# Optimization experiments

Measured on AMD Instinct MI355X. Metric: run time of the kernel, lower is better.

## Reference

```python
import jax, jax.numpy as jnp
import numpy as np

B, LAT, HID = 256, 20, 128
G, BIN = 25000, 25       # original_dim, bin_size
C = 7                    # max_cp + 1 copy-number states
GB = G // BIN            # rho head output dim


def setup_inputs() -> dict:
    key = jax.random.key(0)
    ks = jax.random.split(key, 16)
    s = 0.01  # TruncatedNormal(stddev=0.01) init
    return {
        "z": jax.random.normal(ks[0], (B, LAT), jnp.float32),
        "w0": jax.random.normal(ks[1], (LAT, HID), jnp.float32) * s,
        "b0": jnp.zeros((HID,), jnp.float32),
        "g0": jnp.ones((HID,), jnp.float32),
        "be0": jnp.zeros((HID,), jnp.float32),
        "m0": jax.random.normal(ks[2], (HID,), jnp.float32) * 0.1,
        "v0": jax.random.uniform(ks[3], (HID,), jnp.float32, 0.5, 1.5),
        "w1": jax.random.normal(ks[4], (HID, HID), jnp.float32) * s,
        "b1": jnp.zeros((HID,), jnp.float32),
        "g1": jnp.ones((HID,), jnp.float32),
        "be1": jnp.zeros((HID,), jnp.float32),
        "m1": jax.random.normal(ks[5], (HID,), jnp.float32) * 0.1,
        "v1": jax.random.uniform(ks[6], (HID,), jnp.float32, 0.5, 1.5),
        "wr": jax.random.normal(ks[7], (HID, G), jnp.float32) * s,
        "br": jnp.zeros((G,), jnp.float32),
        "wd": jax.random.normal(ks[8], (HID, G), jnp.float32) * s,
        "bd": jnp.zeros((G,), jnp.float32),
        "wrho": jax.random.normal(ks[9], (C, HID, GB), jnp.float32) * s,
        "brho": jnp.zeros((C, GB), jnp.float32),
        "ws": jax.random.normal(ks[10], (G,), jnp.float32) * 0.05,
        "bs": jax.random.normal(ks[11], (G,), jnp.float32) * 0.05,
    }


def reference(z, w0, b0, g0, be0, m0, v0, w1, b1, g1, be1, m1, v1,
              wr, br, wd, bd, wrho, brho, ws, bs):
    BN_EPS = 1e-3
    EPS = 1e-20
    TEMP = 0.1

    def bn(x, gamma, beta, mean, var):
        # inference-mode BatchNormalization(momentum=0.01, epsilon=0.001)
        return (x - mean) * jax.lax.rsqrt(var + BN_EPS) * gamma + beta

    # FullyConnLayer x2: Dense -> BN -> ReLU
    x = jax.nn.relu(bn(z @ w0 + b0, g0, be0, m0, v0))
    x = jax.nn.relu(bn(x @ w1 + b1, g1, be1, m1, v1))

    theta = jnp.exp(x @ wr + br)        # [B, G]
    pi_drop = x @ wd + bd               # [B, G]

    # max_cp+1 rho Dense heads fused into a single batched GEMM -> [C, B, GB]
    rho = jnp.einsum('bh,cho->cbo', x, wrho) + brho[:, None, :]
    rho = jax.nn.softmax(rho, axis=0)   # softmax over copy-number states

    # GumbelSoftmaxSampling: stack(axis=1) -> [B, C, GB]
    rho_b = jnp.transpose(rho, (1, 0, 2))
    gene_rho = jnp.repeat(rho_b, BIN, axis=-1)        # [B, C, G]
    pi = jnp.transpose(gene_rho, (0, 2, 1))           # [B, G, C]

    u = jax.random.uniform(jax.random.key(42), pi.shape, jnp.float32)
    gnoise = -jnp.log(-jnp.log(u + EPS) + EPS)
    y = jax.nn.softmax((jnp.log(pi + EPS) + gnoise) / TEMP, axis=-1)
    y_hard = (y == jnp.max(y, axis=-1, keepdims=True)).astype(jnp.float32)
    y = jax.lax.stop_gradient(y_hard - y) + y         # straight-through

    # multiply by copy-number index matrix and reduce -> expected/sampled copy
    cvals = jnp.arange(C, dtype=jnp.float32)
    sample = jnp.sum(y * cvals, axis=-1)              # [B, G]

    # ScaleLayer: sigmoid(x * w + b)
    mu = jax.nn.sigmoid(sample * ws + bs)             # [B, G]
    return (mu, theta, pi_drop, sample, pi)
```

## Files before the change

### kernel.cpp

```cpp
#include <hip/hip_runtime.h>

#define B 256
#define LAT 20
#define HID 128
#define G 25000
#define GB 1000
#define NC 7

typedef __attribute__((ext_vector_type(8))) short short8;
typedef __attribute__((ext_vector_type(4))) float f32x4;

__device__ __forceinline__ unsigned short f2bf(float f) {
  unsigned int u = __float_as_uint(f);
  u += 0x7fffu + ((u >> 16) & 1u);
  return (unsigned short)(u >> 16);
}

__device__ __forceinline__ unsigned int threefry_xor(unsigned int idx) {
  unsigned int x0 = 0u;
  unsigned int x1 = idx + 42u;
#define TF_R(r) { x0 += x1; x1 = (x1 << r) | (x1 >> (32 - r)); x1 ^= x0; }
  TF_R(13) TF_R(15) TF_R(26) TF_R(6)
  x0 += 42u;          x1 += 0x1BD11BF1u;
  TF_R(17) TF_R(29) TF_R(16) TF_R(24)
  x0 += 0x1BD11BF0u;  x1 += 2u;
  TF_R(13) TF_R(15) TF_R(26) TF_R(6)
   x1 += 45u;
  TF_R(17) TF_R(29) TF_R(16) TF_R(24)
  x0 += 42u;          x1 += 0x1BD11BF4u;
  TF_R(13) TF_R(15) TF_R(26) TF_R(6)
  x0 += 0x1BD11BF0u;  x1 += 5u;
#undef TF_R
  return x0 ^ x1;
}

__global__ void k_mlp(const float* __restrict__ z,  const float* __restrict__ w0,
                      const float* __restrict__ b0, const float* __restrict__ g0,
                      const float* __restrict__ be0, const float* __restrict__ m0,
                      const float* __restrict__ v0,
                      const float* __restrict__ w1, const float* __restrict__ b1,
                      const float* __restrict__ g1, const float* __restrict__ be1,
                      const float* __restrict__ m1, const float* __restrict__ v1,
                      double* __restrict__ x64, unsigned short* __restrict__ x_bf) {
  __shared__ double xs[HID];
  const int b = blockIdx.x, h = threadIdx.x;
  double acc = (double)b0[h];
  for (int k = 0; k < LAT; ++k)
    acc += (double)z[b * LAT + k] * (double)w0[k * HID + h];
  double y = (acc - (double)m0[h]) * (1.0 / sqrt((double)v0[h] + 1e-3)) * (double)g0[h]
             + (double)be0[h];
  y = y > 0.0 ? y : 0.0;
  xs[h] = y;
  __syncthreads();
  double a1 = (double)b1[h];
  for (int k = 0; k < HID; ++k)
    a1 += xs[k] * (double)w1[k * HID + h];
  double y1 = (a1 - (double)m1[h]) * (1.0 / sqrt((double)v1[h] + 1e-3)) * (double)g1[h]
              + (double)be1[h];
  y1 = y1 > 0.0 ? y1 : 0.0;
  x64[h * B + b] = y1;
  x_bf[b * HID + h] = f2bf((float)y1);
}

__global__ void k_trans(const float* __restrict__ wr, const float* __restrict__ wd,
                        unsigned short* __restrict__ wrT, unsigned short* __restrict__ wdT) {
  __shared__ float t[64][65];
  const float* src = blockIdx.z ? wd : wr;
  unsigned short* dst = blockIdx.z ? wdT : wrT;
  const int g0 = blockIdx.x * 64, h0 = blockIdx.y * 64;
#pragma unroll
  for (int i = 0; i < 16; ++i) {
    int f = i * 256 + threadIdx.x;
    int hl = f >> 6, gl = f & 63;
    int g = g0 + gl;
    t[hl][gl] = (g < G) ? src[(h0 + hl) * G + g] : 0.f;
  }
  __syncthreads();
#pragma unroll
  for (int i = 0; i < 16; ++i) {
    int f = i * 256 + threadIdx.x;
    int gl = f >> 6, hl = f & 63;
    int g = g0 + gl;
    if (g < G) dst[(size_t)g * HID + h0 + hl] = f2bf(t[hl][gl]);
  }
}

__global__ void k_rho(const double* __restrict__ x64, const float* __restrict__ wrho,
                      const float* __restrict__ brho,
                      float* __restrict__ pi32, float* __restrict__ lp32,
                      double* __restrict__ lp64) {
  __shared__ float wl[NC * HID * 16];
  const int o0 = blockIdx.x * 16, bB = blockIdx.y * 64;
  for (int i = threadIdx.x; i < NC * HID * 16; i += 256) {
    int ol = i & 15, hh = (i >> 4) & 127, c = i >> 11;
    int o = o0 + ol;
    wl[i] = (o < GB) ? wrho[(c * HID + hh) * GB + o] : 0.f;
  }
  __syncthreads();
  const int lane = threadIdx.x & 63, w = threadIdx.x >> 6;
  const int b = bB + lane;
  double acc[4][NC];
#pragma unroll
  for (int p = 0; p < 4; ++p) {
    int o = o0 + w + 4 * p; int oc = o < GB ? o : GB - 1;
#pragma unroll
    for (int c = 0; c < NC; ++c) acc[p][c] = (double)brho[c * GB + oc];
  }
  for (int h = 0; h < HID; ++h) {
    double xv = x64[h * B + b];
#pragma unroll
    for (int p = 0; p < 4; ++p) {
#pragma unroll
      for (int c = 0; c < NC; ++c)
        acc[p][c] += xv * (double)wl[(c * HID + h) * 16 + (w + 4 * p)];
    }
  }
#pragma unroll
  for (int p = 0; p < 4; ++p) {
    int o = o0 + w + 4 * p;
    if (o >= GB) continue;
    double m = acc[p][0];
#pragma unroll
    for (int c = 1; c < NC; ++c) m = fmax(m, acc[p][c]);
    double e[NC], s = 0.0;
#pragma unroll
    for (int c = 0; c < NC; ++c) { e[c] = exp(acc[p][c] - m); s += e[c]; }
    size_t base = ((size_t)o * B + b) * 8;
#pragma unroll
    for (int c = 0; c < NC; ++c) {
      double pi = e[c] / s;
      double lp = log(pi + 1e-20);
      pi32[base + c] = (float)pi;
      lp32[base + c] = (float)lp;
      lp64[base + c] = lp;
    }
  }
}

__global__ __launch_bounds__(256) void k_main(
    const unsigned short* __restrict__ x_bf,
    const unsigned short* __restrict__ wrT, const unsigned short* __restrict__ wdT,
    const float* __restrict__ br, const float* __restrict__ bd,
    const float* __restrict__ wsc, const float* __restrict__ bsc,
    const float* __restrict__ pi32, const float* __restrict__ lp32,
    const double* __restrict__ lp64, float* __restrict__ out) {
  const int tid = threadIdx.x;
  const int wv = tid >> 6, lane = tid & 63;
  const int n = lane & 15, quad = lane >> 4;
  const int gt = wv & 1, btbase = (wv >> 1) * 8;
  const int g = blockIdx.x * 32 + gt * 16 + n;
  const bool gvalid = g < G;
  const int gcl = gvalid ? g : G - 1;
  const float brv = br[gcl], bdv = bd[gcl], wsv = wsc[gcl], bsv = bsc[gcl];
  const int o = gcl / 25;
  const float* lpb = lp32 + ((size_t)o * B) * 8;
  const float* pib = pi32 + ((size_t)o * B) * 8;
  const double* lqb = lp64 + ((size_t)o * B) * 8;

  short8 fr[4], fd[4];
  {
    const short8* p1 = (const short8*)(wrT + (size_t)gcl * HID + quad * 8);
    const short8* p2 = (const short8*)(wdT + (size_t)gcl * HID + quad * 8);
#pragma unroll
    for (int ks = 0; ks < 4; ++ks) { fr[ks] = p1[ks * 4]; fd[ks] = p2[ks * 4]; }
  }

  for (int bti = 0; bti < 8; ++bti) {
    const int bt = btbase + bti;
    const short8* xp = (const short8*)(x_bf + (size_t)(bt * 16 + n) * HID + quad * 8);
    f32x4 accr = {0.f, 0.f, 0.f, 0.f}, accd = {0.f, 0.f, 0.f, 0.f};
#pragma unroll
    for (int ks = 0; ks < 4; ++ks) {
      short8 fa = xp[ks * 4];
      accr = __builtin_amdgcn_mfma_f32_16x16x32_bf16(fa, fr[ks], accr, 0, 0, 0);
      accd = __builtin_amdgcn_mfma_f32_16x16x32_bf16(fa, fd[ks], accd, 0, 0, 0);
    }
#pragma unroll
    for (int i = 0; i < 4; ++i) {
      const int b = bt * 16 + quad * 4 + i;
      const float th = expf(accr[i] + brv);
      const float pd = accd[i] + bdv;
      const float* lpp = lpb + (size_t)b * 8;
      f32x4 l0 = *(const f32x4*)lpp;
      f32x4 l1 = *(const f32x4*)(lpp + 4);
      float lpv[8];
      lpv[0] = l0[0]; lpv[1] = l0[1]; lpv[2] = l0[2]; lpv[3] = l0[3];
      lpv[4] = l1[0]; lpv[5] = l1[1]; lpv[6] = l1[2]; lpv[7] = l1[3];
      unsigned int bits[NC];
      const unsigned int idx0 = (unsigned int)b * 175000u + (unsigned int)g * 7u;
      float best = -3.4e38f, sec = -3.4e38f; int arg = 0;
#pragma unroll
      for (int c = 0; c < NC; ++c) {
        unsigned int bb = threefry_xor(idx0 + (unsigned int)c);
        bits[c] = bb;
        float uf = __uint_as_float((bb >> 9) | 0x3f800000u) - 1.0f;
        float gn = -logf(-logf(uf + 1e-20f) + 1e-20f);
        float mv = lpv[c] + gn;
        if (mv > best) { sec = best; best = mv; arg = c; }
        else if (mv > sec) sec = mv;
      }
      int s = arg;
      if (best - sec < 2e-3f) {
        const double* lq = lqb + (size_t)b * 8;
        double lv[NC], bestd = -1e300;
#pragma unroll
        for (int c = 0; c < NC; ++c) {
          float uf = __uint_as_float((bits[c] >> 9) | 0x3f800000u) - 1.0f;
          double gn = -log(-log((double)uf + 1e-20) + 1e-20);
          lv[c] = lq[c] + gn;
          bestd = fmax(bestd, lv[c]);
        }
        s = 0;
#pragma unroll
        for (int c = 0; c < NC; ++c) if (lv[c] == bestd) s += c;
      }
      if (gvalid) {
        const float smp = (float)s;
        const float mu = 1.f / (1.f + expf(-(smp * wsv + bsv)));
        const size_t og = (size_t)b * G + g;
        out[og] = mu;
        out[6400000 + og] = th;
        out[12800000 + og] = pd;
        out[19200000 + og] = smp;
        const float* pip = pib + (size_t)b * 8;
        f32x4 p0 = *(const f32x4*)pip;
        f32x4 p1v = *(const f32x4*)(pip + 4);
        const size_t pbo = 25600000 + og * 7;
        out[pbo + 0] = p0[0]; out[pbo + 1] = p0[1]; out[pbo + 2] = p0[2]; out[pbo + 3] = p0[3];
        out[pbo + 4] = p1v[0]; out[pbo + 5] = p1v[1]; out[pbo + 6] = p1v[2];
      }
    }
  }
}

extern "C" void kernel_launch(void* const* d_in, const int* in_sizes, int n_in,
                              void* d_out, int out_size, void* d_ws, size_t ws_size,
                              hipStream_t stream) {
  const float* z   = (const float*)d_in[0];
  const float* w0  = (const float*)d_in[1];
  const float* b0  = (const float*)d_in[2];
  const float* g0  = (const float*)d_in[3];
  const float* be0 = (const float*)d_in[4];
  const float* m0  = (const float*)d_in[5];
  const float* v0  = (const float*)d_in[6];
  const float* w1  = (const float*)d_in[7];
  const float* b1  = (const float*)d_in[8];
  const float* g1  = (const float*)d_in[9];
  const float* be1 = (const float*)d_in[10];
  const float* m1  = (const float*)d_in[11];
  const float* v1  = (const float*)d_in[12];
  const float* wr  = (const float*)d_in[13];
  const float* br  = (const float*)d_in[14];
  const float* wd  = (const float*)d_in[15];
  const float* bd  = (const float*)d_in[16];
  const float* wrho= (const float*)d_in[17];
  const float* brho= (const float*)d_in[18];
  const float* wsc = (const float*)d_in[19];
  const float* bsc = (const float*)d_in[20];

  char* ws = (char*)d_ws;
  unsigned short* x_bf = (unsigned short*)(ws);
  double* x64          = (double*)(ws + 65536);
  unsigned short* wrT  = (unsigned short*)(ws + 327680);
  unsigned short* wdT  = (unsigned short*)(ws + 6727680);
  float* pi32          = (float*)(ws + 13127680);
  float* lp32          = (float*)(ws + 21319680);
  double* lp64         = (double*)(ws + 29511680);
  float* out = (float*)d_out;

  k_mlp<<<dim3(256), dim3(128), 0, stream>>>(z, w0, b0, g0, be0, m0, v0,
                                             w1, b1, g1, be1, m1, v1, x64, x_bf);
  k_trans<<<dim3(391, 2, 2), dim3(256), 0, stream>>>(wr, wd, wrT, wdT);
  k_rho<<<dim3(63, 4), dim3(256), 0, stream>>>(x64, wrho, brho, pi32, lp32, lp64);
  k_main<<<dim3(782), dim3(256), 0, stream>>>(x_bf, wrT, wdT, br, bd, wsc, bsc,
                                              pi32, lp32, lp64, out);
}
```

Measured before the change: 634.3 us.

## Retile rho and main kernels, switch rho buffers to channel-major layout

k_rho now gives each block 4 output bins instead of 16, so the grid grows from 252 to 1000 blocks and each thread keeps 7 rather than 28 double accumulators. The rho intermediates move from a padded [o][b][8] layout to a channel-major [o][c][b] layout, making the per-channel stores and loads contiguous across batch lanes. k_main adds a second grid dimension that splits the batch tiles, doubling block count and halving the loop per wave. The outer log in the Gumbel noise becomes the fast __logf intrinsic, which may shift near-tie argmax decisions, though a double-precision fallback still handles near ties.

Result: faster. 550.7 us (-13.2%).

```diff
diff --git a/kernel.cpp b/kernel.cpp
--- a/kernel.cpp
+++ b/kernel.cpp
@@ -85,55 +85,43 @@
   }
 }
 
-__global__ void k_rho(const double* __restrict__ x64, const float* __restrict__ wrho,
-                      const float* __restrict__ brho,
+__global__ __launch_bounds__(256) void k_rho(const double* __restrict__ x64,
+                      const float* __restrict__ wrho, const float* __restrict__ brho,
                       float* __restrict__ pi32, float* __restrict__ lp32,
                       double* __restrict__ lp64) {
-  __shared__ float wl[NC * HID * 16];
-  const int o0 = blockIdx.x * 16, bB = blockIdx.y * 64;
-  for (int i = threadIdx.x; i < NC * HID * 16; i += 256) {
-    int ol = i & 15, hh = (i >> 4) & 127, c = i >> 11;
-    int o = o0 + ol;
-    wl[i] = (o < GB) ? wrho[(c * HID + hh) * GB + o] : 0.f;
+  __shared__ float wl[NC * HID * 4];
+  const int o0 = blockIdx.x * 4, bB = blockIdx.y * 64;
+  for (int i = threadIdx.x; i < NC * HID * 4; i += 256) {
+    int ol = i & 3, rest = i >> 2;
+    int c = rest >> 7, h = rest & 127;
+    wl[i] = wrho[(c * HID + h) * GB + o0 + ol];
   }
   __syncthreads();
-  const int lane = threadIdx.x & 63, w = threadIdx.x >> 6;
-  const int b = bB + lane;
-  double acc[4][NC];
-#pragma unroll
-  for (int p = 0; p < 4; ++p) {
-    int o = o0 + w + 4 * p; int oc = o < GB ? o : GB - 1;
-#pragma unroll
-    for (int c = 0; c < NC; ++c) acc[p][c] = (double)brho[c * GB + oc];
-  }
+  const int lane = threadIdx.x & 63, ol = threadIdx.x >> 6;
+  const int b = bB + lane, o = o0 + ol;
+  double acc[NC];
+#pragma unroll
+  for (int c = 0; c < NC; ++c) acc[c] = (double)brho[c * GB + o];
   for (int h = 0; h < HID; ++h) {
     double xv = x64[h * B + b];
 #pragma unroll
-    for (int p = 0; p < 4; ++p) {
-#pragma unroll
-      for (int c = 0; c < NC; ++c)
-        acc[p][c] += xv * (double)wl[(c * HID + h) * 16 + (w + 4 * p)];
-    }
-  }
-#pragma unroll
-  for (int p = 0; p < 4; ++p) {
-    int o = o0 + w + 4 * p;
-    if (o >= GB) continue;
-    double m = acc[p][0];
-#pragma unroll
-    for (int c = 1; c < NC; ++c) m = fmax(m, acc[p][c]);
-    double e[NC], s = 0.0;
-#pragma unroll
-    for (int c = 0; c < NC; ++c) { e[c] = exp(acc[p][c] - m); s += e[c]; }
-    size_t base = ((size_t)o * B + b) * 8;
-#pragma unroll
-    for (int c = 0; c < NC; ++c) {
-      double pi = e[c] / s;
-      double lp = log(pi + 1e-20);
-      pi32[base + c] = (float)pi;
-      lp32[base + c] = (float)lp;
-      lp64[base + c] = lp;
-    }
+    for (int c = 0; c < NC; ++c)
+      acc[c] += xv * (double)wl[(c * HID + h) * 4 + ol];
+  }
+  double m = acc[0];
+#pragma unroll
+  for (int c = 1; c < NC; ++c) m = fmax(m, acc[c]);
+  double e[NC], s = 0.0;
+#pragma unroll
+  for (int c = 0; c < NC; ++c) { e[c] = exp(acc[c] - m); s += e[c]; }
+  const size_t base = (size_t)o * (NC * B) + b;
+#pragma unroll
+  for (int c = 0; c < NC; ++c) {
+    double pi = e[c] / s;
+    double lp = log(pi + 1e-20);
+    pi32[base + c * B] = (float)pi;
+    lp32[base + c * B] = (float)lp;
+    lp64[base + c * B] = lp;
   }
 }
 
@@ -147,15 +135,16 @@
   const int tid = threadIdx.x;
   const int wv = tid >> 6, lane = tid & 63;
   const int n = lane & 15, quad = lane >> 4;
-  const int gt = wv & 1, btbase = (wv >> 1) * 8;
+  const int gt = wv & 1;
+  const int btbase = blockIdx.y * 8 + (wv >> 1) * 4;
   const int g = blockIdx.x * 32 + gt * 16 + n;
   const bool gvalid = g < G;
   const int gcl = gvalid ? g : G - 1;
   const float brv = br[gcl], bdv = bd[gcl], wsv = wsc[gcl], bsv = bsc[gcl];
   const int o = gcl / 25;
-  const float* lpb = lp32 + ((size_t)o * B) * 8;
-  const float* pib = pi32 + ((size_t)o * B) * 8;
-  const double* lqb = lp64 + ((size_t)o * B) * 8;
+  const float*  lpb = lp32 + (size_t)o * (NC * B);
+  const float*  pib = pi32 + (size_t)o * (NC * B);
+  const double* lqb = lp64 + (size_t)o * (NC * B);
 
   short8 fr[4], fd[4];
   {
@@ -165,7 +154,7 @@
     for (int ks = 0; ks < 4; ++ks) { fr[ks] = p1[ks * 4]; fd[ks] = p2[ks * 4]; }
   }
 
-  for (int bti = 0; bti < 8; ++bti) {
+  for (int bti = 0; bti < 4; ++bti) {
     const int bt = btbase + bti;
     const short8* xp = (const short8*)(x_bf + (size_t)(bt * 16 + n) * HID + quad * 8);
     f32x4 accr = {0.f, 0.f, 0.f, 0.f}, accd = {0.f, 0.f, 0.f, 0.f};
@@ -180,12 +169,9 @@
       const int b = bt * 16 + quad * 4 + i;
       const float th = expf(accr[i] + brv);
       const float pd = accd[i] + bdv;
-      const float* lpp = lpb + (size_t)b * 8;
-      f32x4 l0 = *(const f32x4*)lpp;
-      f32x4 l1 = *(const f32x4*)(lpp + 4);
-      float lpv[8];
-      lpv[0] = l0[0]; lpv[1] = l0[1]; lpv[2] = l0[2]; lpv[3] = l0[3];
-      lpv[4] = l1[0]; lpv[5] = l1[1]; lpv[6] = l1[2]; lpv[7] = l1[3];
+      float lpv[NC];
+#pragma unroll
+      for (int c = 0; c < NC; ++c) lpv[c] = lpb[c * B + b];
       unsigned int bits[NC];
       const unsigned int idx0 = (unsigned int)b * 175000u + (unsigned int)g * 7u;
       float best = -3.4e38f, sec = -3.4e38f; int arg = 0;
@@ -194,20 +180,20 @@
         unsigned int bb = threefry_xor(idx0 + (unsigned int)c);
         bits[c] = bb;
         float uf = __uint_as_float((bb >> 9) | 0x3f800000u) - 1.0f;
-        float gn = -logf(-logf(uf + 1e-20f) + 1e-20f);
+        float l1 = -logf(uf + 1e-20f);
+        float gn = -__logf(l1 + 1e-20f);
         float mv = lpv[c] + gn;
         if (mv > best) { sec = best; best = mv; arg = c; }
         else if (mv > sec) sec = mv;
       }
       int s = arg;
       if (best - sec < 2e-3f) {
-        const double* lq = lqb + (size_t)b * 8;
         double lv[NC], bestd = -1e300;
 #pragma unroll
         for (int c = 0; c < NC; ++c) {
           float uf = __uint_as_float((bits[c] >> 9) | 0x3f800000u) - 1.0f;
           double gn = -log(-log((double)uf + 1e-20) + 1e-20);
-          lv[c] = lq[c] + gn;
+          lv[c] = lqb[c * B + b] + gn;
           bestd = fmax(bestd, lv[c]);
         }
         s = 0;
@@ -222,12 +208,9 @@
         out[6400000 + og] = th;
         out[12800000 + og] = pd;
         out[19200000 + og] = smp;
-        const float* pip = pib + (size_t)b * 8;
-        f32x4 p0 = *(const f32x4*)pip;
-        f32x4 p1v = *(const f32x4*)(pip + 4);
         const size_t pbo = 25600000 + og * 7;
-        out[pbo + 0] = p0[0]; out[pbo + 1] = p0[1]; out[pbo + 2] = p0[2]; out[pbo + 3] = p0[3];
-        out[pbo + 4] = p1v[0]; out[pbo + 5] = p1v[1]; out[pbo + 6] = p1v[2];
+#pragma unroll
+        for (int c = 0; c < NC; ++c) out[pbo + c] = pib[c * B + b];
       }
     }
   }
@@ -264,14 +247,14 @@
   unsigned short* wrT  = (unsigned short*)(ws + 327680);
   unsigned short* wdT  = (unsigned short*)(ws + 6727680);
   float* pi32          = (float*)(ws + 13127680);
-  float* lp32          = (float*)(ws + 21319680);
-  double* lp64         = (double*)(ws + 29511680);
+  float* lp32          = (float*)(ws + 20295680);
+  double* lp64         = (double*)(ws + 27463680);
   float* out = (float*)d_out;
 
   k_mlp<<<dim3(256), dim3(128), 0, stream>>>(z, w0, b0, g0, be0, m0, v0,
                                              w1, b1, g1, be1, m1, v1, x64, x_bf);
   k_trans<<<dim3(391, 2, 2), dim3(256), 0, stream>>>(wr, wd, wrT, wdT);
-  k_rho<<<dim3(63, 4), dim3(256), 0, stream>>>(x64, wrho, brho, pi32, lp32, lp64);
-  k_main<<<dim3(782), dim3(256), 0, stream>>>(x_bf, wrT, wdT, br, bd, wsc, bsc,
-                                              pi32, lp32, lp64, out);
-}
+  k_rho<<<dim3(250, 4), dim3(256), 0, stream>>>(x64, wrho, brho, pi32, lp32, lp64);
+  k_main<<<dim3(782, 2), dim3(256), 0, stream>>>(x_bf, wrT, wdT, br, bd, wsc, bsc,
+                                                 pi32, lp32, lp64, out);
+}
```
